# Optimization experiments

Hardware: AMD Instinct MI355X
Metric: run time of the kernel (lower is better)

Reference implementation:

```python
import jax, jax.numpy as jnp
import numpy as np

V_MIN = -10.0
V_MAX = 10.0
N_ATOMS = 101
LN_EPS = 1e-5

B = 131072
N_OBS = 60
N_ACT = 20
H = 256


def _layer_norm(x, g, b):
    mu = jnp.mean(x, axis=-1, keepdims=True)
    var = jnp.mean(jnp.square(x - mu), axis=-1, keepdims=True)
    return (x - mu) * jax.lax.rsqrt(var + LN_EPS) * g + b


def _mlp(x, W1, b1, g1, be1, W2, b2, g2, be2, W3, b3, g3, be3, W4, b4):
    h = jax.nn.silu(_layer_norm(x @ W1 + b1, g1, be1))
    h = jax.nn.silu(_layer_norm(h @ W2 + b2, g2, be2))
    h = jax.nn.silu(_layer_norm(h @ W3 + b3, g3, be3))
    return h @ W4 + b4  # [B, N_ATOMS] logits


def setup_inputs() -> dict:
    key = jax.random.key(0)
    ks = jax.random.split(key, 10)
    s = 0.05
    return {
        'obs': jax.random.normal(ks[0], (B, N_OBS), jnp.float32),
        'actions': jax.random.normal(ks[1], (B, N_ACT), jnp.float32),
        'rewards': jax.random.normal(ks[2], (B,), jnp.float32),
        'bootstrap': jax.random.uniform(ks[3], (B,), jnp.float32),
        'discount': jax.random.uniform(ks[4], (B,), jnp.float32, 0.95, 0.99),
        'q_support': jnp.linspace(V_MIN, V_MAX, N_ATOMS, dtype=jnp.float32),
        'W1': jax.random.normal(ks[5], (N_OBS + N_ACT, H), jnp.float32) * s,
        'b1': jnp.zeros((H,), jnp.float32),
        'g1': jnp.ones((H,), jnp.float32),
        'be1': jnp.zeros((H,), jnp.float32),
        'W2': jax.random.normal(ks[6], (H, H // 2), jnp.float32) * s,
        'b2': jnp.zeros((H // 2,), jnp.float32),
        'g2': jnp.ones((H // 2,), jnp.float32),
        'be2': jnp.zeros((H // 2,), jnp.float32),
        'W3': jax.random.normal(ks[7], (H // 2, H // 4), jnp.float32) * s,
        'b3': jnp.zeros((H // 4,), jnp.float32),
        'g3': jnp.ones((H // 4,), jnp.float32),
        'be3': jnp.zeros((H // 4,), jnp.float32),
        'W4': jax.random.normal(ks[8], (H // 4, N_ATOMS), jnp.float32) * s,
        'b4': jnp.zeros((N_ATOMS,), jnp.float32),
    }


def reference(obs, actions, rewards, bootstrap, discount, q_support,
              W1, b1, g1, be1, W2, b2, g2, be2, W3, b3, g3, be3, W4, b4):
    batch = rewards.shape[0]
    delta_z = (V_MAX - V_MIN) / (N_ATOMS - 1)
    # Bellman target support: [B, N_ATOMS]
    target_z = rewards[:, None] + bootstrap[:, None] * discount[:, None] * q_support
    target_z = jnp.clip(target_z, V_MIN, V_MAX)
    b = (target_z - V_MIN) / delta_z
    li = jnp.floor(b).astype(jnp.int32)
    ui = jnp.ceil(b).astype(jnp.int32)
    is_int = ui == li
    lower_mask = is_int & (li > 0)
    upper_mask = is_int & (li == 0)
    li = jnp.where(lower_mask, li - 1, li)
    ui = jnp.where(upper_mask, ui + 1, ui)
    lf = li.astype(b.dtype)
    uf = ui.astype(b.dtype)

    x = jnp.concatenate([obs, actions], axis=-1)
    logits = _mlp(x, W1, b1, g1, be1, W2, b2, g2, be2, W3, b3, g3, be3, W4, b4)
    next_dist = jax.nn.softmax(logits, axis=1)

    size = batch * N_ATOMS
    offset = (jnp.arange(batch, dtype=jnp.int32) * N_ATOMS)[:, None]
    l_idx = jnp.clip((li + offset).reshape(-1), 0, size - 1)
    u_idx = jnp.clip((ui + offset).reshape(-1), 0, size - 1)
    lw = (next_dist * (uf - b)).reshape(-1)
    uw = (next_dist * (b - lf)).reshape(-1)
    proj = jnp.zeros((size,), next_dist.dtype).at[l_idx].add(lw).at[u_idx].add(uw)
    return proj.reshape(batch, N_ATOMS)
```

## Files before the change

kernel.cpp:

```cpp
#include <hip/hip_runtime.h>
#include <math.h>

typedef __bf16 bf16x8 __attribute__((ext_vector_type(8)));
typedef float f32x4 __attribute__((ext_vector_type(4)));

__global__ void conv_weights(const float* __restrict__ W1, const float* __restrict__ W2,
                             const float* __restrict__ W3, const float* __restrict__ W4,
                             __bf16* __restrict__ ws)
{
  const int f = blockIdx.x * 4 + (threadIdx.x >> 6);
  const int lane = threadIdx.x & 63;
  int f0, ntot, Ksrc, Nsrc, off;
  const float* W;
  if (f < 48)       { f0 = f;       ntot = 16; Ksrc = 80;  Nsrc = 256; W = W1; off = 0; }
  else if (f < 112) { f0 = f - 48;  ntot = 8;  Ksrc = 256; Nsrc = 128; W = W2; off = 24576; }
  else if (f < 128) { f0 = f - 112; ntot = 4;  Ksrc = 128; Nsrc = 64;  W = W3; off = 57344; }
  else              { f0 = f - 128; ntot = 8;  Ksrc = 64;  Nsrc = 101; W = W4; off = 65536; }
  const int kt = f0 / ntot, nt = f0 % ntot;
  const int q = lane >> 4, c = lane & 15;
  const int n = nt * 16 + c;
  bf16x8 v;
#pragma unroll
  for (int j = 0; j < 8; ++j) {
    const int k = kt * 32 + q * 8 + j;
    const float x = (k < Ksrc && n < Nsrc) ? W[k * Nsrc + n] : 0.f;
    v[j] = (__bf16)x;
  }
  ((bf16x8*)(ws + off))[f0 * 64 + lane] = v;
}


__global__ __launch_bounds__(256, 3)
void sacq_wave(const float* __restrict__ obs,  const float* __restrict__ act,
               const float* __restrict__ rew,  const float* __restrict__ boot,
               const float* __restrict__ disc, const float* __restrict__ qsup,
               const float* __restrict__ b1, const float* __restrict__ g1, const float* __restrict__ be1,
               const float* __restrict__ b2, const float* __restrict__ g2, const float* __restrict__ be2,
               const float* __restrict__ b3, const float* __restrict__ g3, const float* __restrict__ be3,
               const float* __restrict__ b4,
               const __bf16* __restrict__ ws,
               float* __restrict__ out)
{
  __shared__ float sm[8768];
  const int t = threadIdx.x;
  const int wv = t >> 6, lane = t & 63;
  const int q = lane >> 4, c = lane & 15;
  float* smw = sm + wv * 2192;
  __bf16* h1 = (__bf16*)smw;
  __bf16* h2 = (__bf16*)smw;
  __bf16* h3 = (__bf16*)smw;
  float*  proj = smw + 576;
  const int row0w = blockIdx.x * 64 + wv * 16;
  const bf16x8* wsf = (const bf16x8*)ws;

  f32x4 acc1[16];
  {
    bf16x8 A1[3];
    const float4* ob4 = (const float4*)(obs + (size_t)(row0w + c) * 60);
    const float4* ac4 = (const float4*)(act + (size_t)(row0w + c) * 20);
#pragma unroll
    for (int kt = 0; kt < 3; ++kt) {
      const int k0 = kt * 32 + q * 8;
      float v[8];
      if (k0 < 56) {
        const float4 a = ob4[k0 / 4], b = ob4[k0 / 4 + 1];
        v[0]=a.x; v[1]=a.y; v[2]=a.z; v[3]=a.w; v[4]=b.x; v[5]=b.y; v[6]=b.z; v[7]=b.w;
      } else if (k0 == 56) {
        const float4 a = ob4[14], b = ac4[0];
        v[0]=a.x; v[1]=a.y; v[2]=a.z; v[3]=a.w; v[4]=b.x; v[5]=b.y; v[6]=b.z; v[7]=b.w;
      } else if (k0 < 80) {
        const float4 a = ac4[(k0 - 60) / 4], b = ac4[(k0 - 60) / 4 + 1];
        v[0]=a.x; v[1]=a.y; v[2]=a.z; v[3]=a.w; v[4]=b.x; v[5]=b.y; v[6]=b.z; v[7]=b.w;
      } else {
#pragma unroll
        for (int j = 0; j < 8; ++j) v[j] = 0.f;
      }
#pragma unroll
      for (int j = 0; j < 8; ++j) A1[kt][j] = (__bf16)v[j];
    }
#pragma unroll
    for (int nt = 0; nt < 16; ++nt) {
      const float bb = b1[nt * 16 + c];
      f32x4 vv = {bb, bb, bb, bb};
      acc1[nt] = vv;
    }
#pragma unroll
    for (int ch = 0; ch < 4; ++ch) {
      bf16x8 Bb[3][4];
#pragma unroll
      for (int kt = 0; kt < 3; ++kt)
#pragma unroll
        for (int j = 0; j < 4; ++j)
          Bb[kt][j] = wsf[(kt * 16 + ch * 4 + j) * 64 + lane];
#pragma unroll
      for (int kt = 0; kt < 3; ++kt)
#pragma unroll
        for (int j = 0; j < 4; ++j)
          acc1[ch * 4 + j] = __builtin_amdgcn_mfma_f32_16x16x32_bf16(A1[kt], Bb[kt][j], acc1[ch * 4 + j], 0, 0, 0);
    }
    float mu[4], rs[4];
#pragma unroll
    for (int r = 0; r < 4; ++r) {
      float s = 0.f, s2 = 0.f;
#pragma unroll
      for (int nt = 0; nt < 16; ++nt) { const float v = acc1[nt][r]; s += v; s2 += v * v; }
      s += __shfl_xor(s, 1); s2 += __shfl_xor(s2, 1);
      s += __shfl_xor(s, 2); s2 += __shfl_xor(s2, 2);
      s += __shfl_xor(s, 4); s2 += __shfl_xor(s2, 4);
      s += __shfl_xor(s, 8); s2 += __shfl_xor(s2, 8);
      const float m = s * (1.f / 256.f);
      mu[r] = m;
      rs[r] = rsqrtf(s2 * (1.f / 256.f) - m * m + 1e-5f);
    }
#pragma unroll
    for (int nt = 0; nt < 16; ++nt) {
      const int col = nt * 16 + c;
      const float gg = g1[col], bb = be1[col];
#pragma unroll
      for (int r = 0; r < 4; ++r) {
        float v = (acc1[nt][r] - mu[r]) * rs[r] * gg + bb;
        v = v * __builtin_amdgcn_rcpf(1.f + __expf(-v));
        h1[(4 * q + r) * 264 + col] = (__bf16)v;
      }
    }
  }

  {
    f32x4 acc2[8];
#pragma unroll
    for (int nt = 0; nt < 8; ++nt) {
      const float bb = b2[nt * 16 + c];
      f32x4 vv = {bb, bb, bb, bb};
      acc2[nt] = vv;
    }
    bf16x8 B2[3][8];
#pragma unroll
    for (int nt = 0; nt < 8; ++nt) B2[0][nt] = wsf[3072 + (0 * 8 + nt) * 64 + lane];
#pragma unroll
    for (int nt = 0; nt < 8; ++nt) B2[1][nt] = wsf[3072 + (1 * 8 + nt) * 64 + lane];
#pragma unroll
    for (int kt = 0; kt < 8; ++kt) {
      if (kt + 2 < 8) {
#pragma unroll
        for (int nt = 0; nt < 8; ++nt)
          B2[(kt + 2) % 3][nt] = wsf[3072 + ((kt + 2) * 8 + nt) * 64 + lane];
      }
      const bf16x8 A2 = *(const bf16x8*)(h1 + c * 264 + kt * 32 + q * 8);
#pragma unroll
      for (int nt = 0; nt < 8; ++nt)
        acc2[nt] = __builtin_amdgcn_mfma_f32_16x16x32_bf16(A2, B2[kt % 3][nt], acc2[nt], 0, 0, 0);
    }
    float mu[4], rs[4];
#pragma unroll
    for (int r = 0; r < 4; ++r) {
      float s = 0.f, s2 = 0.f;
#pragma unroll
      for (int nt = 0; nt < 8; ++nt) { const float v = acc2[nt][r]; s += v; s2 += v * v; }
      s += __shfl_xor(s, 1); s2 += __shfl_xor(s2, 1);
      s += __shfl_xor(s, 2); s2 += __shfl_xor(s2, 2);
      s += __shfl_xor(s, 4); s2 += __shfl_xor(s2, 4);
      s += __shfl_xor(s, 8); s2 += __shfl_xor(s2, 8);
      const float m = s * (1.f / 128.f);
      mu[r] = m;
      rs[r] = rsqrtf(s2 * (1.f / 128.f) - m * m + 1e-5f);
    }
#pragma unroll
    for (int nt = 0; nt < 8; ++nt) {
      const int col = nt * 16 + c;
      const float gg = g2[col], bb = be2[col];
#pragma unroll
      for (int r = 0; r < 4; ++r) {
        float v = (acc2[nt][r] - mu[r]) * rs[r] * gg + bb;
        v = v * __builtin_amdgcn_rcpf(1.f + __expf(-v));
        h2[(4 * q + r) * 136 + col] = (__bf16)v;
      }
    }
  }

  {
    bf16x8 B3[4][4];
#pragma unroll
    for (int kt = 0; kt < 4; ++kt)
#pragma unroll
      for (int nt = 0; nt < 4; ++nt)
        B3[kt][nt] = wsf[7168 + (kt * 4 + nt) * 64 + lane];
    f32x4 acc3[4];
#pragma unroll
    for (int nt = 0; nt < 4; ++nt) {
      const float bb = b3[nt * 16 + c];
      f32x4 vv = {bb, bb, bb, bb};
      acc3[nt] = vv;
    }
#pragma unroll
    for (int kt = 0; kt < 4; ++kt) {
      const bf16x8 A3 = *(const bf16x8*)(h2 + c * 136 + kt * 32 + q * 8);
#pragma unroll
      for (int nt = 0; nt < 4; ++nt)
        acc3[nt] = __builtin_amdgcn_mfma_f32_16x16x32_bf16(A3, B3[kt][nt], acc3[nt], 0, 0, 0);
    }
    float mu[4], rs[4];
#pragma unroll
    for (int r = 0; r < 4; ++r) {
      float s = 0.f, s2 = 0.f;
#pragma unroll
      for (int nt = 0; nt < 4; ++nt) { const float v = acc3[nt][r]; s += v; s2 += v * v; }
      s += __shfl_xor(s, 1); s2 += __shfl_xor(s2, 1);
      s += __shfl_xor(s, 2); s2 += __shfl_xor(s2, 2);
      s += __shfl_xor(s, 4); s2 += __shfl_xor(s2, 4);
      s += __shfl_xor(s, 8); s2 += __shfl_xor(s2, 8);
      const float m = s * (1.f / 64.f);
      mu[r] = m;
      rs[r] = rsqrtf(s2 * (1.f / 64.f) - m * m + 1e-5f);
    }
#pragma unroll
    for (int nt = 0; nt < 4; ++nt) {
      const int col = nt * 16 + c;
      const float gg = g3[col], bb = be3[col];
#pragma unroll
      for (int r = 0; r < 4; ++r) {
        float v = (acc3[nt][r] - mu[r]) * rs[r] * gg + bb;
        v = v * __builtin_amdgcn_rcpf(1.f + __expf(-v));
        h3[(4 * q + r) * 72 + col] = (__bf16)v;
      }
    }
  }

  {
    bf16x8 B4[2][7];
#pragma unroll
    for (int kt = 0; kt < 2; ++kt)
#pragma unroll
      for (int nt = 0; nt < 7; ++nt)
        B4[kt][nt] = wsf[8192 + (kt * 8 + nt) * 64 + lane];
    bf16x8 A4f[2];
#pragma unroll
    for (int kt = 0; kt < 2; ++kt)
      A4f[kt] = *(const bf16x8*)(h3 + c * 72 + kt * 32 + q * 8);

    asm volatile("" ::: "memory");
    {
      f32x4 z = {0.f, 0.f, 0.f, 0.f};
      f32x4* p4 = (f32x4*)proj;
      for (int i = lane; i < 404; i += 64) p4[i] = z;
    }

    f32x4 a4[7];
#pragma unroll
    for (int nt = 0; nt < 7; ++nt) {
      const int col = nt * 16 + c;
      const float bb = (col < 101) ? b4[col] : 0.f;
      f32x4 vv = {bb, bb, bb, bb};
      a4[nt] = vv;
    }
#pragma unroll
    for (int kt = 0; kt < 2; ++kt) {
#pragma unroll
      for (int nt = 0; nt < 7; ++nt)
        a4[nt] = __builtin_amdgcn_mfma_f32_16x16x32_bf16(A4f[kt], B4[kt][nt], a4[nt], 0, 0, 0);
    }

    float mx4[4] = {-3.4e38f, -3.4e38f, -3.4e38f, -3.4e38f};
#pragma unroll
    for (int nt = 0; nt < 7; ++nt) {
      const bool ok = (nt < 6) | (c < 5);
#pragma unroll
      for (int r = 0; r < 4; ++r)
        if (ok) mx4[r] = fmaxf(mx4[r], a4[nt][r]);
    }
#pragma unroll
    for (int r = 0; r < 4; ++r) {
      mx4[r] = fmaxf(mx4[r], __shfl_xor(mx4[r], 1));
      mx4[r] = fmaxf(mx4[r], __shfl_xor(mx4[r], 2));
      mx4[r] = fmaxf(mx4[r], __shfl_xor(mx4[r], 4));
      mx4[r] = fmaxf(mx4[r], __shfl_xor(mx4[r], 8));
    }
    float sm4[4] = {0.f, 0.f, 0.f, 0.f};
#pragma unroll
    for (int nt = 0; nt < 7; ++nt) {
      const bool ok = (nt < 6) | (c < 5);
#pragma unroll
      for (int r = 0; r < 4; ++r) {
        const float e = ok ? __expf(a4[nt][r] - mx4[r]) : 0.f;
        a4[nt][r] = e;
        sm4[r] += e;
      }
    }
    float inv4[4];
#pragma unroll
    for (int r = 0; r < 4; ++r) {
      float s = sm4[r];
      s += __shfl_xor(s, 1);
      s += __shfl_xor(s, 2);
      s += __shfl_xor(s, 4);
      s += __shfl_xor(s, 8);
      inv4[r] = __builtin_amdgcn_rcpf(s);
    }

    float rwv[4], bdv[4];
#pragma unroll
    for (int r = 0; r < 4; ++r) {
      const int gr = row0w + 4 * q + r;
      rwv[r] = rew[gr];
      bdv[r] = boot[gr] * disc[gr];
    }

#pragma unroll
    for (int nt = 0; nt < 7; ++nt) {
      const int col = nt * 16 + c;
      if ((nt < 6) | (c < 5)) {
        const float qsv = qsup[col];
#pragma unroll
        for (int r = 0; r < 4; ++r) {
          const float p = a4[nt][r] * inv4[r];
          float tz = rwv[r] + bdv[r] * qsv;
          tz = fminf(fmaxf(tz, -10.f), 10.f);
          const float b_ = (tz + 10.f) * 5.f;
          const float fl = floorf(b_), cl = ceilf(b_);
          int li = (int)fl, ui = (int)cl;
          if (ui == li) { if (li > 0) --li; else ++ui; }
          const int rb = (4 * q + r) * 101;
          atomicAdd(&proj[rb + li], p * ((float)ui - b_));
          atomicAdd(&proj[rb + ui], p * (b_ - (float)li));
        }
      }
    }
  }

  {
    const f32x4* p4 = (const f32x4*)proj;
    f32x4* o4 = (f32x4*)(out + (size_t)row0w * 101);
    for (int i = lane; i < 404; i += 64) o4[i] = p4[i];
  }
}

extern "C" void kernel_launch(void* const* d_in, const int* in_sizes, int n_in,
                              void* d_out, int out_size, void* d_ws, size_t ws_size,
                              hipStream_t stream)
{
  const int B = in_sizes[2];
  __bf16* ws = (__bf16*)d_ws;

  conv_weights<<<dim3(36), dim3(256), 0, stream>>>(
      (const float*)d_in[6], (const float*)d_in[10], (const float*)d_in[14],
      (const float*)d_in[18], ws);

  sacq_wave<<<dim3(B / 64), dim3(256), 0, stream>>>(
      (const float*)d_in[0],  (const float*)d_in[1],  (const float*)d_in[2],
      (const float*)d_in[3],  (const float*)d_in[4],  (const float*)d_in[5],
      (const float*)d_in[7],  (const float*)d_in[8],  (const float*)d_in[9],
      (const float*)d_in[11], (const float*)d_in[12], (const float*)d_in[13],
      (const float*)d_in[15], (const float*)d_in[16], (const float*)d_in[17],
      (const float*)d_in[19], ws, (float*)d_out);
}
```

Baseline: 323.2 us.

## Transpose MFMA accumulators through LDS for vectorized LayerNorm/SiLU/softmax epilogues

Each wave now spills its MFMA accumulator tiles into a per-wave LDS scratch buffer in a transposed layout. Lanes then reread them so each lane handles four rows of one column, with mean and rstd shared through LDS, instead of each lane covering four rows across many column tiles. The bias, gamma, beta and q_support vectors are packed into the workspace by an extra block of the weight-conversion kernel, and rewards, bootstrap and discount are read as float4. The aim is to cut register pressure and per-element broadcast loads in the epilogues. The cost is LDS traffic, a doubled shared-memory footprint and a drop of the launch-bounds occupancy hint from 3 to 2 blocks per CU.

```diff
diff --git a/kernel.cpp b/kernel.cpp
--- a/kernel.cpp
+++ b/kernel.cpp
@@ -6,8 +6,32 @@
 
 __global__ void conv_weights(const float* __restrict__ W1, const float* __restrict__ W2,
                              const float* __restrict__ W3, const float* __restrict__ W4,
+                             const float* __restrict__ b1, const float* __restrict__ g1, const float* __restrict__ be1,
+                             const float* __restrict__ b2, const float* __restrict__ g2, const float* __restrict__ be2,
+                             const float* __restrict__ b3, const float* __restrict__ g3, const float* __restrict__ be3,
+                             const float* __restrict__ b4, const float* __restrict__ qsup,
                              __bf16* __restrict__ ws)
 {
+  if (blockIdx.x == 36) {
+    float* Pp = (float*)(ws + 73728);
+    const int t = threadIdx.x;
+    Pp[t]       = b1[t];
+    Pp[256 + t] = g1[t];
+    Pp[512 + t] = be1[t];
+    if (t < 128) {
+      Pp[768 + t]  = b2[t];
+      Pp[896 + t]  = g2[t];
+      Pp[1024 + t] = be2[t];
+      Pp[1344 + t] = (t < 101) ? b4[t]   : 0.f;
+      Pp[1472 + t] = (t < 101) ? qsup[t] : 0.f;
+    }
+    if (t < 64) {
+      Pp[1152 + t] = b3[t];
+      Pp[1216 + t] = g3[t];
+      Pp[1280 + t] = be3[t];
+    }
+    return;
+  }
   const int f = blockIdx.x * 4 + (threadIdx.x >> 6);
   const int lane = threadIdx.x & 63;
   int f0, ntot, Ksrc, Nsrc, off;
@@ -30,7 +54,7 @@
 }
 
 
-__global__ __launch_bounds__(256, 3)
+__global__ __launch_bounds__(256, 2)
 void sacq_wave(const float* __restrict__ obs,  const float* __restrict__ act,
                const float* __restrict__ rew,  const float* __restrict__ boot,
                const float* __restrict__ disc, const float* __restrict__ qsup,
@@ -41,17 +65,21 @@
                const __bf16* __restrict__ ws,
                float* __restrict__ out)
 {
-  __shared__ float sm[8768];
+  __shared__ float sm[16960];
   const int t = threadIdx.x;
   const int wv = t >> 6, lane = t & 63;
   const int q = lane >> 4, c = lane & 15;
-  float* smw = sm + wv * 2192;
-  __bf16* h1 = (__bf16*)smw;
-  __bf16* h2 = (__bf16*)smw;
-  __bf16* h3 = (__bf16*)smw;
-  float*  proj = smw + 576;
+  float* smw = sm + wv * 4240;
+  float* scr = smw;
+  __bf16* h = (__bf16*)(smw + 2048);
+  float* muL = smw + 4160;
+  float* rsL = smw + 4176;
+  float* proj = smw + 2624;
   const int row0w = blockIdx.x * 64 + wv * 16;
   const bf16x8* wsf = (const bf16x8*)ws;
+  const float* Pp = (const float*)(const void*)(ws + 73728);
+  const int lq = lane >> 2;
+  const int lr = (lane & 3) * 4;
 
   f32x4 acc1[16];
   {
@@ -80,7 +108,7 @@
     }
 #pragma unroll
     for (int nt = 0; nt < 16; ++nt) {
-      const float bb = b1[nt * 16 + c];
+      const float bb = Pp[nt * 16 + c];
       f32x4 vv = {bb, bb, bb, bb};
       acc1[nt] = vv;
     }
@@ -98,29 +126,39 @@
         for (int j = 0; j < 4; ++j)
           acc1[ch * 4 + j] = __builtin_amdgcn_mfma_f32_16x16x32_bf16(A1[kt], Bb[kt][j], acc1[ch * 4 + j], 0, 0, 0);
     }
-    float mu[4], rs[4];
+    float s[4] = {0.f,0.f,0.f,0.f}, s2[4] = {0.f,0.f,0.f,0.f};
+#pragma unroll
+    for (int nt = 0; nt < 16; ++nt)
+#pragma unroll
+      for (int r = 0; r < 4; ++r) { const float v = acc1[nt][r]; s[r] += v; s2[r] += v * v; }
 #pragma unroll
     for (int r = 0; r < 4; ++r) {
-      float s = 0.f, s2 = 0.f;
-#pragma unroll
-      for (int nt = 0; nt < 16; ++nt) { const float v = acc1[nt][r]; s += v; s2 += v * v; }
-      s += __shfl_xor(s, 1); s2 += __shfl_xor(s2, 1);
-      s += __shfl_xor(s, 2); s2 += __shfl_xor(s2, 2);
-      s += __shfl_xor(s, 4); s2 += __shfl_xor(s2, 4);
-      s += __shfl_xor(s, 8); s2 += __shfl_xor(s2, 8);
-      const float m = s * (1.f / 256.f);
-      mu[r] = m;
-      rs[r] = rsqrtf(s2 * (1.f / 256.f) - m * m + 1e-5f);
-    }
-#pragma unroll
-    for (int nt = 0; nt < 16; ++nt) {
-      const int col = nt * 16 + c;
-      const float gg = g1[col], bb = be1[col];
-#pragma unroll
-      for (int r = 0; r < 4; ++r) {
-        float v = (acc1[nt][r] - mu[r]) * rs[r] * gg + bb;
-        v = v * __builtin_amdgcn_rcpf(1.f + __expf(-v));
-        h1[(4 * q + r) * 264 + col] = (__bf16)v;
+      s[r] += __shfl_xor(s[r], 1); s2[r] += __shfl_xor(s2[r], 1);
+      s[r] += __shfl_xor(s[r], 2); s2[r] += __shfl_xor(s2[r], 2);
+      s[r] += __shfl_xor(s[r], 4); s2[r] += __shfl_xor(s2[r], 4);
+      s[r] += __shfl_xor(s[r], 8); s2[r] += __shfl_xor(s2[r], 8);
+      const float m = s[r] * (1.f / 256.f);
+      const float rv = rsqrtf(s2[r] * (1.f / 256.f) - m * m + 1e-5f);
+      if (c == 0) { muL[4 * q + r] = m; rsL[4 * q + r] = rv; }
+    }
+#pragma unroll
+    for (int hh = 0; hh < 2; ++hh) {
+#pragma unroll
+      for (int ntl = 0; ntl < 8; ++ntl)
+        *(f32x4*)(scr + (ntl * 16 + c) * 16 + 4 * q) = acc1[hh * 8 + ntl];
+#pragma unroll 1
+      for (int it = 0; it < 8; ++it) {
+        const int colh = it * 16 + lq, col = hh * 128 + colh;
+        const f32x4 v  = *(const f32x4*)(scr + colh * 16 + lr);
+        const f32x4 m  = *(const f32x4*)(muL + lr);
+        const f32x4 rv = *(const f32x4*)(rsL + lr);
+        const float gg = Pp[256 + col], bb = Pp[512 + col];
+#pragma unroll
+        for (int j = 0; j < 4; ++j) {
+          float x = (v[j] - m[j]) * rv[j] * gg + bb;
+          x = x * __builtin_amdgcn_rcpf(1.f + __expf(-x));
+          h[(lr + j) * 264 + col] = (__bf16)x;
+        }
       }
     }
   }
@@ -129,7 +167,7 @@
     f32x4 acc2[8];
 #pragma unroll
     for (int nt = 0; nt < 8; ++nt) {
-      const float bb = b2[nt * 16 + c];
+      const float bb = Pp[768 + nt * 16 + c];
       f32x4 vv = {bb, bb, bb, bb};
       acc2[nt] = vv;
     }
@@ -145,34 +183,41 @@
         for (int nt = 0; nt < 8; ++nt)
           B2[(kt + 2) % 3][nt] = wsf[3072 + ((kt + 2) * 8 + nt) * 64 + lane];
       }
-      const bf16x8 A2 = *(const bf16x8*)(h1 + c * 264 + kt * 32 + q * 8);
+      const bf16x8 A2 = *(const bf16x8*)(h + c * 264 + kt * 32 + q * 8);
 #pragma unroll
       for (int nt = 0; nt < 8; ++nt)
         acc2[nt] = __builtin_amdgcn_mfma_f32_16x16x32_bf16(A2, B2[kt % 3][nt], acc2[nt], 0, 0, 0);
     }
-    float mu[4], rs[4];
+    float s[4] = {0.f,0.f,0.f,0.f}, s2[4] = {0.f,0.f,0.f,0.f};
+#pragma unroll
+    for (int nt = 0; nt < 8; ++nt)
+#pragma unroll
+      for (int r = 0; r < 4; ++r) { const float v = acc2[nt][r]; s[r] += v; s2[r] += v * v; }
 #pragma unroll
     for (int r = 0; r < 4; ++r) {
-      float s = 0.f, s2 = 0.f;
-#pragma unroll
-      for (int nt = 0; nt < 8; ++nt) { const float v = acc2[nt][r]; s += v; s2 += v * v; }
-      s += __shfl_xor(s, 1); s2 += __shfl_xor(s2, 1);
-      s += __shfl_xor(s, 2); s2 += __shfl_xor(s2, 2);
-      s += __shfl_xor(s, 4); s2 += __shfl_xor(s2, 4);
-      s += __shfl_xor(s, 8); s2 += __shfl_xor(s2, 8);
-      const float m = s * (1.f / 128.f);
-      mu[r] = m;
-      rs[r] = rsqrtf(s2 * (1.f / 128.f) - m * m + 1e-5f);
-    }
-#pragma unroll
-    for (int nt = 0; nt < 8; ++nt) {
-      const int col = nt * 16 + c;
-      const float gg = g2[col], bb = be2[col];
-#pragma unroll
-      for (int r = 0; r < 4; ++r) {
-        float v = (acc2[nt][r] - mu[r]) * rs[r] * gg + bb;
-        v = v * __builtin_amdgcn_rcpf(1.f + __expf(-v));
-        h2[(4 * q + r) * 136 + col] = (__bf16)v;
+      s[r] += __shfl_xor(s[r], 1); s2[r] += __shfl_xor(s2[r], 1);
+      s[r] += __shfl_xor(s[r], 2); s2[r] += __shfl_xor(s2[r], 2);
+      s[r] += __shfl_xor(s[r], 4); s2[r] += __shfl_xor(s2[r], 4);
+      s[r] += __shfl_xor(s[r], 8); s2[r] += __shfl_xor(s2[r], 8);
+      const float m = s[r] * (1.f / 128.f);
+      const float rv = rsqrtf(s2[r] * (1.f / 128.f) - m * m + 1e-5f);
+      if (c == 0) { muL[4 * q + r] = m; rsL[4 * q + r] = rv; }
+    }
+#pragma unroll
+    for (int nt = 0; nt < 8; ++nt)
+      *(f32x4*)(scr + (nt * 16 + c) * 16 + 4 * q) = acc2[nt];
+#pragma unroll 1
+    for (int it = 0; it < 8; ++it) {
+      const int col = it * 16 + lq;
+      const f32x4 v  = *(const f32x4*)(scr + col * 16 + lr);
+      const f32x4 m  = *(const f32x4*)(muL + lr);
+      const f32x4 rv = *(const f32x4*)(rsL + lr);
+      const float gg = Pp[896 + col], bb = Pp[1024 + col];
+#pragma unroll
+      for (int j = 0; j < 4; ++j) {
+        float x = (v[j] - m[j]) * rv[j] * gg + bb;
+        x = x * __builtin_amdgcn_rcpf(1.f + __expf(-x));
+        h[(lr + j) * 136 + col] = (__bf16)x;
       }
     }
   }
@@ -187,40 +232,47 @@
     f32x4 acc3[4];
 #pragma unroll
     for (int nt = 0; nt < 4; ++nt) {
-      const float bb = b3[nt * 16 + c];
+      const float bb = Pp[1152 + nt * 16 + c];
       f32x4 vv = {bb, bb, bb, bb};
       acc3[nt] = vv;
     }
 #pragma unroll
     for (int kt = 0; kt < 4; ++kt) {
-      const bf16x8 A3 = *(const bf16x8*)(h2 + c * 136 + kt * 32 + q * 8);
+      const bf16x8 A3 = *(const bf16x8*)(h + c * 136 + kt * 32 + q * 8);
 #pragma unroll
       for (int nt = 0; nt < 4; ++nt)
         acc3[nt] = __builtin_amdgcn_mfma_f32_16x16x32_bf16(A3, B3[kt][nt], acc3[nt], 0, 0, 0);
     }
-    float mu[4], rs[4];
+    float s[4] = {0.f,0.f,0.f,0.f}, s2[4] = {0.f,0.f,0.f,0.f};
+#pragma unroll
+    for (int nt = 0; nt < 4; ++nt)
+#pragma unroll
+      for (int r = 0; r < 4; ++r) { const float v = acc3[nt][r]; s[r] += v; s2[r] += v * v; }
 #pragma unroll
     for (int r = 0; r < 4; ++r) {
-      float s = 0.f, s2 = 0.f;
-#pragma unroll
-      for (int nt = 0; nt < 4; ++nt) { const float v = acc3[nt][r]; s += v; s2 += v * v; }
-      s += __shfl_xor(s, 1); s2 += __shfl_xor(s2, 1);
-      s += __shfl_xor(s, 2); s2 += __shfl_xor(s2, 2);
-      s += __shfl_xor(s, 4); s2 += __shfl_xor(s2, 4);
-      s += __shfl_xor(s, 8); s2 += __shfl_xor(s2, 8);
-      const float m = s * (1.f / 64.f);
-      mu[r] = m;
-      rs[r] = rsqrtf(s2 * (1.f / 64.f) - m * m + 1e-5f);
-    }
-#pragma unroll
-    for (int nt = 0; nt < 4; ++nt) {
-      const int col = nt * 16 + c;
-      const float gg = g3[col], bb = be3[col];
-#pragma unroll
-      for (int r = 0; r < 4; ++r) {
-        float v = (acc3[nt][r] - mu[r]) * rs[r] * gg + bb;
-        v = v * __builtin_amdgcn_rcpf(1.f + __expf(-v));
-        h3[(4 * q + r) * 72 + col] = (__bf16)v;
+      s[r] += __shfl_xor(s[r], 1); s2[r] += __shfl_xor(s2[r], 1);
+      s[r] += __shfl_xor(s[r], 2); s2[r] += __shfl_xor(s2[r], 2);
+      s[r] += __shfl_xor(s[r], 4); s2[r] += __shfl_xor(s2[r], 4);
+      s[r] += __shfl_xor(s[r], 8); s2[r] += __shfl_xor(s2[r], 8);
+      const float m = s[r] * (1.f / 64.f);
+      const float rv = rsqrtf(s2[r] * (1.f / 64.f) - m * m + 1e-5f);
+      if (c == 0) { muL[4 * q + r] = m; rsL[4 * q + r] = rv; }
+    }
+#pragma unroll
+    for (int nt = 0; nt < 4; ++nt)
+      *(f32x4*)(scr + (nt * 16 + c) * 16 + 4 * q) = acc3[nt];
+#pragma unroll 1
+    for (int it = 0; it < 4; ++it) {
+      const int col = it * 16 + lq;
+      const f32x4 v  = *(const f32x4*)(scr + col * 16 + lr);
+      const f32x4 m  = *(const f32x4*)(muL + lr);
+      const f32x4 rv = *(const f32x4*)(rsL + lr);
+      const float gg = Pp[1216 + col], bb = Pp[1280 + col];
+#pragma unroll
+      for (int j = 0; j < 4; ++j) {
+        float x = (v[j] - m[j]) * rv[j] * gg + bb;
+        x = x * __builtin_amdgcn_rcpf(1.f + __expf(-x));
+        h[(lr + j) * 72 + col] = (__bf16)x;
       }
     }
   }
@@ -235,7 +287,23 @@
     bf16x8 A4f[2];
 #pragma unroll
     for (int kt = 0; kt < 2; ++kt)
-      A4f[kt] = *(const bf16x8*)(h3 + c * 72 + kt * 32 + q * 8);
+      A4f[kt] = *(const bf16x8*)(h + c * 72 + kt * 32 + q * 8);
+    f32x4 a4[7];
+#pragma unroll
+    for (int nt = 0; nt < 7; ++nt) {
+      const float bb = Pp[1344 + nt * 16 + c];
+      f32x4 vv = {bb, bb, bb, bb};
+      a4[nt] = vv;
+    }
+#pragma unroll
+    for (int kt = 0; kt < 2; ++kt) {
+#pragma unroll
+      for (int nt = 0; nt < 7; ++nt)
+        a4[nt] = __builtin_amdgcn_mfma_f32_16x16x32_bf16(A4f[kt], B4[kt][nt], a4[nt], 0, 0, 0);
+    }
+#pragma unroll
+    for (int nt = 0; nt < 7; ++nt)
+      *(f32x4*)(scr + (nt * 16 + c) * 16 + 4 * q) = a4[nt];
 
     asm volatile("" ::: "memory");
     {
@@ -244,81 +312,66 @@
       for (int i = lane; i < 404; i += 64) p4[i] = z;
     }
 
-    f32x4 a4[7];
-#pragma unroll
-    for (int nt = 0; nt < 7; ++nt) {
-      const int col = nt * 16 + c;
-      const float bb = (col < 101) ? b4[col] : 0.f;
-      f32x4 vv = {bb, bb, bb, bb};
-      a4[nt] = vv;
-    }
-#pragma unroll
-    for (int kt = 0; kt < 2; ++kt) {
-#pragma unroll
-      for (int nt = 0; nt < 7; ++nt)
-        a4[nt] = __builtin_amdgcn_mfma_f32_16x16x32_bf16(A4f[kt], B4[kt][nt], a4[nt], 0, 0, 0);
-    }
-
-    float mx4[4] = {-3.4e38f, -3.4e38f, -3.4e38f, -3.4e38f};
-#pragma unroll
-    for (int nt = 0; nt < 7; ++nt) {
-      const bool ok = (nt < 6) | (c < 5);
-#pragma unroll
-      for (int r = 0; r < 4; ++r)
-        if (ok) mx4[r] = fmaxf(mx4[r], a4[nt][r]);
-    }
-#pragma unroll
-    for (int r = 0; r < 4; ++r) {
-      mx4[r] = fmaxf(mx4[r], __shfl_xor(mx4[r], 1));
-      mx4[r] = fmaxf(mx4[r], __shfl_xor(mx4[r], 2));
-      mx4[r] = fmaxf(mx4[r], __shfl_xor(mx4[r], 4));
-      mx4[r] = fmaxf(mx4[r], __shfl_xor(mx4[r], 8));
-    }
-    float sm4[4] = {0.f, 0.f, 0.f, 0.f};
-#pragma unroll
-    for (int nt = 0; nt < 7; ++nt) {
-      const bool ok = (nt < 6) | (c < 5);
-#pragma unroll
-      for (int r = 0; r < 4; ++r) {
-        const float e = ok ? __expf(a4[nt][r] - mx4[r]) : 0.f;
-        a4[nt][r] = e;
-        sm4[r] += e;
-      }
-    }
-    float inv4[4];
-#pragma unroll
-    for (int r = 0; r < 4; ++r) {
-      float s = sm4[r];
-      s += __shfl_xor(s, 1);
-      s += __shfl_xor(s, 2);
-      s += __shfl_xor(s, 4);
-      s += __shfl_xor(s, 8);
-      inv4[r] = __builtin_amdgcn_rcpf(s);
-    }
-
-    float rwv[4], bdv[4];
-#pragma unroll
-    for (int r = 0; r < 4; ++r) {
-      const int gr = row0w + 4 * q + r;
-      rwv[r] = rew[gr];
-      bdv[r] = boot[gr] * disc[gr];
-    }
-
-#pragma unroll
-    for (int nt = 0; nt < 7; ++nt) {
-      const int col = nt * 16 + c;
-      if ((nt < 6) | (c < 5)) {
-        const float qsv = qsup[col];
-#pragma unroll
-        for (int r = 0; r < 4; ++r) {
-          const float p = a4[nt][r] * inv4[r];
-          float tz = rwv[r] + bdv[r] * qsv;
+    float mx[4] = {-3.4e38f, -3.4e38f, -3.4e38f, -3.4e38f};
+#pragma unroll 1
+    for (int it = 0; it < 7; ++it) {
+      const int col = it * 16 + lq;
+      const f32x4 v = *(const f32x4*)(scr + col * 16 + lr);
+      if (col < 101) {
+#pragma unroll
+        for (int j = 0; j < 4; ++j) mx[j] = fmaxf(mx[j], v[j]);
+      }
+    }
+#pragma unroll
+    for (int j = 0; j < 4; ++j) {
+      mx[j] = fmaxf(mx[j], __shfl_xor(mx[j], 4));
+      mx[j] = fmaxf(mx[j], __shfl_xor(mx[j], 8));
+      mx[j] = fmaxf(mx[j], __shfl_xor(mx[j], 16));
+      mx[j] = fmaxf(mx[j], __shfl_xor(mx[j], 32));
+    }
+    float sp[4] = {0.f, 0.f, 0.f, 0.f};
+#pragma unroll 1
+    for (int it = 0; it < 7; ++it) {
+      const int col = it * 16 + lq;
+      const f32x4 v = *(const f32x4*)(scr + col * 16 + lr);
+      const bool ok = col < 101;
+#pragma unroll
+      for (int j = 0; j < 4; ++j) sp[j] += ok ? __expf(v[j] - mx[j]) : 0.f;
+    }
+    float inv[4];
+#pragma unroll
+    for (int j = 0; j < 4; ++j) {
+      float x = sp[j];
+      x += __shfl_xor(x, 4);
+      x += __shfl_xor(x, 8);
+      x += __shfl_xor(x, 16);
+      x += __shfl_xor(x, 32);
+      inv[j] = __builtin_amdgcn_rcpf(x);
+    }
+
+    const f32x4 rw4 = *(const f32x4*)(rew  + row0w + lr);
+    const f32x4 bo4 = *(const f32x4*)(boot + row0w + lr);
+    const f32x4 di4 = *(const f32x4*)(disc + row0w + lr);
+    float bd[4];
+#pragma unroll
+    for (int j = 0; j < 4; ++j) bd[j] = bo4[j] * di4[j];
+
+#pragma unroll 1
+    for (int it = 0; it < 7; ++it) {
+      const int col = it * 16 + lq;
+      if (col < 101) {
+        const float qsv = Pp[1472 + col];
+        const f32x4 v = *(const f32x4*)(scr + col * 16 + lr);
+#pragma unroll
+        for (int j = 0; j < 4; ++j) {
+          const float p = __expf(v[j] - mx[j]) * inv[j];
+          float tz = rw4[j] + bd[j] * qsv;
           tz = fminf(fmaxf(tz, -10.f), 10.f);
           const float b_ = (tz + 10.f) * 5.f;
           const float fl = floorf(b_), cl = ceilf(b_);
           int li = (int)fl, ui = (int)cl;
           if (ui == li) { if (li > 0) --li; else ++ui; }
-          const int rb = (4 * q + r) * 101;
+          const int rb = (lr + j) * 101;
           atomicAdd(&proj[rb + li], p * ((float)ui - b_));
           atomicAdd(&proj[rb + ui], p * (b_ - (float)li));
         }
@@ -340,9 +393,13 @@
   const int B = in_sizes[2];
   __bf16* ws = (__bf16*)d_ws;
 
-  conv_weights<<<dim3(36), dim3(256), 0, stream>>>(
-      (const float*)d_in[6], (const float*)d_in[10], (const float*)d_in[14],
-      (const float*)d_in[18], ws);
+  conv_weights<<<dim3(37), dim3(256), 0, stream>>>(
+      (const float*)d_in[6],  (const float*)d_in[10], (const float*)d_in[14],
+      (const float*)d_in[18],
+      (const float*)d_in[7],  (const float*)d_in[8],  (const float*)d_in[9],
+      (const float*)d_in[11], (const float*)d_in[12], (const float*)d_in[13],
+      (const float*)d_in[15], (const float*)d_in[16], (const float*)d_in[17],
+      (const float*)d_in[19], (const float*)d_in[5],  ws);
 
   sacq_wave<<<dim3(B / 64), dim3(256), 0, stream>>>(
       (const float*)d_in[0],  (const float*)d_in[1],  (const float*)d_in[2],
```

Result: slower. 344.9 us (+6.7%).

## Process two 16-row tiles per wave to reuse weight fragments across rows

Applied to the files above, without the earlier changes.

Each wave now handles 32 rows (two 16-row MFMA tiles), so every weight B-fragment loaded from global memory feeds two MFMAs, which halves weight traffic per row. Bias, LayerNorm and q_support parameters are packed into the workspace by an extra block of the prep kernel. Reward, bootstrap and discount are read as vectors. LDS per block doubles, register pressure rises and launch bounds drop to 2 blocks per CU, so occupancy and latency hiding may suffer.

```diff
diff --git a/kernel.cpp b/kernel.cpp
--- a/kernel.cpp
+++ b/kernel.cpp
@@ -6,8 +6,32 @@
 
 __global__ void conv_weights(const float* __restrict__ W1, const float* __restrict__ W2,
                              const float* __restrict__ W3, const float* __restrict__ W4,
+                             const float* __restrict__ b1, const float* __restrict__ g1, const float* __restrict__ be1,
+                             const float* __restrict__ b2, const float* __restrict__ g2, const float* __restrict__ be2,
+                             const float* __restrict__ b3, const float* __restrict__ g3, const float* __restrict__ be3,
+                             const float* __restrict__ b4, const float* __restrict__ qsup,
                              __bf16* __restrict__ ws)
 {
+  if (blockIdx.x == 36) {
+    float* Pp = (float*)(ws + 73728);
+    const int t = threadIdx.x;
+    Pp[t]       = b1[t];
+    Pp[256 + t] = g1[t];
+    Pp[512 + t] = be1[t];
+    if (t < 128) {
+      Pp[768 + t]  = b2[t];
+      Pp[896 + t]  = g2[t];
+      Pp[1024 + t] = be2[t];
+      Pp[1344 + t] = (t < 101) ? b4[t]   : 0.f;
+      Pp[1472 + t] = (t < 101) ? qsup[t] : 0.f;
+    }
+    if (t < 64) {
+      Pp[1152 + t] = b3[t];
+      Pp[1216 + t] = g3[t];
+      Pp[1280 + t] = be3[t];
+    }
+    return;
+  }
   const int f = blockIdx.x * 4 + (threadIdx.x >> 6);
   const int lane = threadIdx.x & 63;
   int f0, ntot, Ksrc, Nsrc, off;
@@ -30,7 +54,7 @@
 }
 
 
-__global__ __launch_bounds__(256, 3)
+__global__ __launch_bounds__(256, 2)
 void sacq_wave(const float* __restrict__ obs,  const float* __restrict__ act,
                const float* __restrict__ rew,  const float* __restrict__ boot,
                const float* __restrict__ disc, const float* __restrict__ qsup,
@@ -41,48 +65,51 @@
                const __bf16* __restrict__ ws,
                float* __restrict__ out)
 {
-  __shared__ float sm[8768];
+  __shared__ float sm[17536];
   const int t = threadIdx.x;
   const int wv = t >> 6, lane = t & 63;
   const int q = lane >> 4, c = lane & 15;
-  float* smw = sm + wv * 2192;
-  __bf16* h1 = (__bf16*)smw;
-  __bf16* h2 = (__bf16*)smw;
-  __bf16* h3 = (__bf16*)smw;
-  float*  proj = smw + 576;
-  const int row0w = blockIdx.x * 64 + wv * 16;
+  float* smw = sm + wv * 4384;
+  __bf16* h = (__bf16*)smw;
+  float* proj = smw + 1152;
+  const int row0w = blockIdx.x * 128 + wv * 32;
   const bf16x8* wsf = (const bf16x8*)ws;
-
-  f32x4 acc1[16];
+  const float* Pp = (const float*)(const void*)(ws + 73728);
+
+  f32x4 acc1[2][16];
   {
-    bf16x8 A1[3];
-    const float4* ob4 = (const float4*)(obs + (size_t)(row0w + c) * 60);
-    const float4* ac4 = (const float4*)(act + (size_t)(row0w + c) * 20);
-#pragma unroll
-    for (int kt = 0; kt < 3; ++kt) {
-      const int k0 = kt * 32 + q * 8;
-      float v[8];
-      if (k0 < 56) {
-        const float4 a = ob4[k0 / 4], b = ob4[k0 / 4 + 1];
-        v[0]=a.x; v[1]=a.y; v[2]=a.z; v[3]=a.w; v[4]=b.x; v[5]=b.y; v[6]=b.z; v[7]=b.w;
-      } else if (k0 == 56) {
-        const float4 a = ob4[14], b = ac4[0];
-        v[0]=a.x; v[1]=a.y; v[2]=a.z; v[3]=a.w; v[4]=b.x; v[5]=b.y; v[6]=b.z; v[7]=b.w;
-      } else if (k0 < 80) {
-        const float4 a = ac4[(k0 - 60) / 4], b = ac4[(k0 - 60) / 4 + 1];
-        v[0]=a.x; v[1]=a.y; v[2]=a.z; v[3]=a.w; v[4]=b.x; v[5]=b.y; v[6]=b.z; v[7]=b.w;
-      } else {
-#pragma unroll
-        for (int j = 0; j < 8; ++j) v[j] = 0.f;
-      }
-#pragma unroll
-      for (int j = 0; j < 8; ++j) A1[kt][j] = (__bf16)v[j];
+    bf16x8 A1[2][3];
+#pragma unroll
+    for (int rt = 0; rt < 2; ++rt) {
+      const float4* ob4 = (const float4*)(obs + (size_t)(row0w + rt * 16 + c) * 60);
+      const float4* ac4 = (const float4*)(act + (size_t)(row0w + rt * 16 + c) * 20);
+#pragma unroll
+      for (int kt = 0; kt < 3; ++kt) {
+        const int k0 = kt * 32 + q * 8;
+        float v[8];
+        if (k0 < 56) {
+          const float4 a = ob4[k0 / 4], b = ob4[k0 / 4 + 1];
+          v[0]=a.x; v[1]=a.y; v[2]=a.z; v[3]=a.w; v[4]=b.x; v[5]=b.y; v[6]=b.z; v[7]=b.w;
+        } else if (k0 == 56) {
+          const float4 a = ob4[14], b = ac4[0];
+          v[0]=a.x; v[1]=a.y; v[2]=a.z; v[3]=a.w; v[4]=b.x; v[5]=b.y; v[6]=b.z; v[7]=b.w;
+        } else if (k0 < 80) {
+          const float4 a = ac4[(k0 - 60) / 4], b = ac4[(k0 - 60) / 4 + 1];
+          v[0]=a.x; v[1]=a.y; v[2]=a.z; v[3]=a.w; v[4]=b.x; v[5]=b.y; v[6]=b.z; v[7]=b.w;
+        } else {
+#pragma unroll
+          for (int j = 0; j < 8; ++j) v[j] = 0.f;
+        }
+#pragma unroll
+        for (int j = 0; j < 8; ++j) A1[rt][kt][j] = (__bf16)v[j];
+      }
     }
 #pragma unroll
     for (int nt = 0; nt < 16; ++nt) {
-      const float bb = b1[nt * 16 + c];
+      const float bb = Pp[nt * 16 + c];
       f32x4 vv = {bb, bb, bb, bb};
-      acc1[nt] = vv;
+      acc1[0][nt] = vv;
+      acc1[1][nt] = vv;
     }
 #pragma unroll
     for (int ch = 0; ch < 4; ++ch) {
@@ -96,83 +123,99 @@
       for (int kt = 0; kt < 3; ++kt)
 #pragma unroll
         for (int j = 0; j < 4; ++j)
-          acc1[ch * 4 + j] = __builtin_amdgcn_mfma_f32_16x16x32_bf16(A1[kt], Bb[kt][j], acc1[ch * 4 + j], 0, 0, 0);
-    }
-    float mu[4], rs[4];
-#pragma unroll
-    for (int r = 0; r < 4; ++r) {
-      float s = 0.f, s2 = 0.f;
-#pragma unroll
-      for (int nt = 0; nt < 16; ++nt) { const float v = acc1[nt][r]; s += v; s2 += v * v; }
-      s += __shfl_xor(s, 1); s2 += __shfl_xor(s2, 1);
-      s += __shfl_xor(s, 2); s2 += __shfl_xor(s2, 2);
-      s += __shfl_xor(s, 4); s2 += __shfl_xor(s2, 4);
-      s += __shfl_xor(s, 8); s2 += __shfl_xor(s2, 8);
-      const float m = s * (1.f / 256.f);
-      mu[r] = m;
-      rs[r] = rsqrtf(s2 * (1.f / 256.f) - m * m + 1e-5f);
-    }
-#pragma unroll
-    for (int nt = 0; nt < 16; ++nt) {
-      const int col = nt * 16 + c;
-      const float gg = g1[col], bb = be1[col];
+#pragma unroll
+          for (int rt = 0; rt < 2; ++rt)
+            acc1[rt][ch * 4 + j] = __builtin_amdgcn_mfma_f32_16x16x32_bf16(A1[rt][kt], Bb[kt][j], acc1[rt][ch * 4 + j], 0, 0, 0);
+    }
+#pragma unroll
+    for (int rt = 0; rt < 2; ++rt) {
+      float s[4] = {0.f,0.f,0.f,0.f}, s2[4] = {0.f,0.f,0.f,0.f};
+#pragma unroll
+      for (int nt = 0; nt < 16; ++nt)
+#pragma unroll
+        for (int r = 0; r < 4; ++r) { const float v = acc1[rt][nt][r]; s[r] += v; s2[r] += v * v; }
+      float mu[4], rs[4];
 #pragma unroll
       for (int r = 0; r < 4; ++r) {
-        float v = (acc1[nt][r] - mu[r]) * rs[r] * gg + bb;
-        v = v * __builtin_amdgcn_rcpf(1.f + __expf(-v));
-        h1[(4 * q + r) * 264 + col] = (__bf16)v;
+        s[r] += __shfl_xor(s[r], 1); s2[r] += __shfl_xor(s2[r], 1);
+        s[r] += __shfl_xor(s[r], 2); s2[r] += __shfl_xor(s2[r], 2);
+        s[r] += __shfl_xor(s[r], 4); s2[r] += __shfl_xor(s2[r], 4);
+        s[r] += __shfl_xor(s[r], 8); s2[r] += __shfl_xor(s2[r], 8);
+        const float m = s[r] * (1.f / 256.f);
+        mu[r] = m;
+        rs[r] = rsqrtf(s2[r] * (1.f / 256.f) - m * m + 1e-5f);
+      }
+#pragma unroll
+      for (int nt = 0; nt < 16; ++nt) {
+        const int col = nt * 16 + c;
+        const float gg = Pp[256 + col], bb = Pp[512 + col];
+#pragma unroll
+        for (int r = 0; r < 4; ++r) {
+          float v = (acc1[rt][nt][r] - mu[r]) * rs[r] * gg + bb;
+          v = v * __builtin_amdgcn_rcpf(1.f + __expf(-v));
+          h[(rt * 16 + 4 * q + r) * 264 + col] = (__bf16)v;
+        }
       }
     }
   }
 
   {
-    f32x4 acc2[8];
+    f32x4 acc2[2][8];
 #pragma unroll
     for (int nt = 0; nt < 8; ++nt) {
-      const float bb = b2[nt * 16 + c];
+      const float bb = Pp[768 + nt * 16 + c];
       f32x4 vv = {bb, bb, bb, bb};
-      acc2[nt] = vv;
-    }
-    bf16x8 B2[3][8];
-#pragma unroll
-    for (int nt = 0; nt < 8; ++nt) B2[0][nt] = wsf[3072 + (0 * 8 + nt) * 64 + lane];
-#pragma unroll
-    for (int nt = 0; nt < 8; ++nt) B2[1][nt] = wsf[3072 + (1 * 8 + nt) * 64 + lane];
+      acc2[0][nt] = vv;
+      acc2[1][nt] = vv;
+    }
+    bf16x8 B2[2][8];
+#pragma unroll
+    for (int nt = 0; nt < 8; ++nt) B2[0][nt] = wsf[3072 + nt * 64 + lane];
 #pragma unroll
     for (int kt = 0; kt < 8; ++kt) {
-      if (kt + 2 < 8) {
+      if (kt + 1 < 8) {
 #pragma unroll
         for (int nt = 0; nt < 8; ++nt)
-          B2[(kt + 2) % 3][nt] = wsf[3072 + ((kt + 2) * 8 + nt) * 64 + lane];
-      }
-      const bf16x8 A2 = *(const bf16x8*)(h1 + c * 264 + kt * 32 + q * 8);
+          B2[(kt + 1) & 1][nt] = wsf[3072 + ((kt + 1) * 8 + nt) * 64 + lane];
+      }
+      bf16x8 A2r[2];
+#pragma unroll
+      for (int rt = 0; rt < 2; ++rt)
+        A2r[rt] = *(const bf16x8*)(h + (rt * 16 + c) * 264 + kt * 32 + q * 8);
 #pragma unroll
       for (int nt = 0; nt < 8; ++nt)
-        acc2[nt] = __builtin_amdgcn_mfma_f32_16x16x32_bf16(A2, B2[kt % 3][nt], acc2[nt], 0, 0, 0);
-    }
-    float mu[4], rs[4];
-#pragma unroll
-    for (int r = 0; r < 4; ++r) {
-      float s = 0.f, s2 = 0.f;
-#pragma unroll
-      for (int nt = 0; nt < 8; ++nt) { const float v = acc2[nt][r]; s += v; s2 += v * v; }
-      s += __shfl_xor(s, 1); s2 += __shfl_xor(s2, 1);
-      s += __shfl_xor(s, 2); s2 += __shfl_xor(s2, 2);
-      s += __shfl_xor(s, 4); s2 += __shfl_xor(s2, 4);
-      s += __shfl_xor(s, 8); s2 += __shfl_xor(s2, 8);
-      const float m = s * (1.f / 128.f);
-      mu[r] = m;
-      rs[r] = rsqrtf(s2 * (1.f / 128.f) - m * m + 1e-5f);
-    }
-#pragma unroll
-    for (int nt = 0; nt < 8; ++nt) {
-      const int col = nt * 16 + c;
-      const float gg = g2[col], bb = be2[col];
+#pragma unroll
+        for (int rt = 0; rt < 2; ++rt)
+          acc2[rt][nt] = __builtin_amdgcn_mfma_f32_16x16x32_bf16(A2r[rt], B2[kt & 1][nt], acc2[rt][nt], 0, 0, 0);
+    }
+#pragma unroll
+    for (int rt = 0; rt < 2; ++rt) {
+      float s[4] = {0.f,0.f,0.f,0.f}, s2[4] = {0.f,0.f,0.f,0.f};
+#pragma unroll
+      for (int nt = 0; nt < 8; ++nt)
+#pragma unroll
+        for (int r = 0; r < 4; ++r) { const float v = acc2[rt][nt][r]; s[r] += v; s2[r] += v * v; }
+      float mu[4], rs[4];
 #pragma unroll
       for (int r = 0; r < 4; ++r) {
-        float v = (acc2[nt][r] - mu[r]) * rs[r] * gg + bb;
-        v = v * __builtin_amdgcn_rcpf(1.f + __expf(-v));
-        h2[(4 * q + r) * 136 + col] = (__bf16)v;
+        s[r] += __shfl_xor(s[r], 1); s2[r] += __shfl_xor(s2[r], 1);
+        s[r] += __shfl_xor(s[r], 2); s2[r] += __shfl_xor(s2[r], 2);
+        s[r] += __shfl_xor(s[r], 4); s2[r] += __shfl_xor(s2[r], 4);
+        s[r] += __shfl_xor(s[r], 8); s2[r] += __shfl_xor(s2[r], 8);
+        const float m = s[r] * (1.f / 128.f);
+        mu[r] = m;
+        rs[r] = rsqrtf(s2[r] * (1.f / 128.f) - m * m + 1e-5f);
+      }
+#pragma unroll
+      for (int nt = 0; nt < 8; ++nt) {
+        const int col = nt * 16 + c;
+        const float gg = Pp[896 + col], bb = Pp[1024 + col];
+#pragma unroll
+        for (int r = 0; r < 4; ++r) {
+          float v = (acc2[rt][nt][r] - mu[r]) * rs[r] * gg + bb;
+          v = v * __builtin_amdgcn_rcpf(1.f + __expf(-v));
+          h[(rt * 16 + 4 * q + r) * 136 + col] = (__bf16)v;
+        }
       }
     }
   }
@@ -184,43 +227,54 @@
 #pragma unroll
       for (int nt = 0; nt < 4; ++nt)
         B3[kt][nt] = wsf[7168 + (kt * 4 + nt) * 64 + lane];
-    f32x4 acc3[4];
+    f32x4 acc3[2][4];
 #pragma unroll
     for (int nt = 0; nt < 4; ++nt) {
-      const float bb = b3[nt * 16 + c];
+      const float bb = Pp[1152 + nt * 16 + c];
       f32x4 vv = {bb, bb, bb, bb};
-      acc3[nt] = vv;
+      acc3[0][nt] = vv;
+      acc3[1][nt] = vv;
     }
 #pragma unroll
     for (int kt = 0; kt < 4; ++kt) {
-      const bf16x8 A3 = *(const bf16x8*)(h2 + c * 136 + kt * 32 + q * 8);
+      bf16x8 A3r[2];
+#pragma unroll
+      for (int rt = 0; rt < 2; ++rt)
+        A3r[rt] = *(const bf16x8*)(h + (rt * 16 + c) * 136 + kt * 32 + q * 8);
 #pragma unroll
       for (int nt = 0; nt < 4; ++nt)
-        acc3[nt] = __builtin_amdgcn_mfma_f32_16x16x32_bf16(A3, B3[kt][nt], acc3[nt], 0, 0, 0);
-    }
-    float mu[4], rs[4];
-#pragma unroll
-    for (int r = 0; r < 4; ++r) {
-      float s = 0.f, s2 = 0.f;
-#pragma unroll
-      for (int nt = 0; nt < 4; ++nt) { const float v = acc3[nt][r]; s += v; s2 += v * v; }
-      s += __shfl_xor(s, 1); s2 += __shfl_xor(s2, 1);
-      s += __shfl_xor(s, 2); s2 += __shfl_xor(s2, 2);
-      s += __shfl_xor(s, 4); s2 += __shfl_xor(s2, 4);
-      s += __shfl_xor(s, 8); s2 += __shfl_xor(s2, 8);
-      const float m = s * (1.f / 64.f);
-      mu[r] = m;
-      rs[r] = rsqrtf(s2 * (1.f / 64.f) - m * m + 1e-5f);
-    }
-#pragma unroll
-    for (int nt = 0; nt < 4; ++nt) {
-      const int col = nt * 16 + c;
-      const float gg = g3[col], bb = be3[col];
+#pragma unroll
+        for (int rt = 0; rt < 2; ++rt)
+          acc3[rt][nt] = __builtin_amdgcn_mfma_f32_16x16x32_bf16(A3r[rt], B3[kt][nt], acc3[rt][nt], 0, 0, 0);
+    }
+#pragma unroll
+    for (int rt = 0; rt < 2; ++rt) {
+      float s[4] = {0.f,0.f,0.f,0.f}, s2[4] = {0.f,0.f,0.f,0.f};
+#pragma unroll
+      for (int nt = 0; nt < 4; ++nt)
+#pragma unroll
+        for (int r = 0; r < 4; ++r) { const float v = acc3[rt][nt][r]; s[r] += v; s2[r] += v * v; }
+      float mu[4], rs[4];
 #pragma unroll
       for (int r = 0; r < 4; ++r) {
-        float v = (acc3[nt][r] - mu[r]) * rs[r] * gg + bb;
-        v = v * __builtin_amdgcn_rcpf(1.f + __expf(-v));
-        h3[(4 * q + r) * 72 + col] = (__bf16)v;
+        s[r] += __shfl_xor(s[r], 1); s2[r] += __shfl_xor(s2[r], 1);
+        s[r] += __shfl_xor(s[r], 2); s2[r] += __shfl_xor(s2[r], 2);
+        s[r] += __shfl_xor(s[r], 4); s2[r] += __shfl_xor(s2[r], 4);
+        s[r] += __shfl_xor(s[r], 8); s2[r] += __shfl_xor(s2[r], 8);
+        const float m = s[r] * (1.f / 64.f);
+        mu[r] = m;
+        rs[r] = rsqrtf(s2[r] * (1.f / 64.f) - m * m + 1e-5f);
+      }
+#pragma unroll
+      for (int nt = 0; nt < 4; ++nt) {
+        const int col = nt * 16 + c;
+        const float gg = Pp[1216 + col], bb = Pp[1280 + col];
+#pragma unroll
+        for (int r = 0; r < 4; ++r) {
+          float v = (acc3[rt][nt][r] - mu[r]) * rs[r] * gg + bb;
+          v = v * __builtin_amdgcn_rcpf(1.f + __expf(-v));
+          h[(rt * 16 + 4 * q + r) * 72 + col] = (__bf16)v;
+        }
       }
     }
   }
@@ -232,95 +286,100 @@
 #pragma unroll
       for (int nt = 0; nt < 7; ++nt)
         B4[kt][nt] = wsf[8192 + (kt * 8 + nt) * 64 + lane];
-    bf16x8 A4f[2];
-#pragma unroll
-    for (int kt = 0; kt < 2; ++kt)
-      A4f[kt] = *(const bf16x8*)(h3 + c * 72 + kt * 32 + q * 8);
+    bf16x8 A4f[2][2];
+#pragma unroll
+    for (int rt = 0; rt < 2; ++rt)
+#pragma unroll
+      for (int kt = 0; kt < 2; ++kt)
+        A4f[rt][kt] = *(const bf16x8*)(h + (rt * 16 + c) * 72 + kt * 32 + q * 8);
 
     asm volatile("" ::: "memory");
     {
       f32x4 z = {0.f, 0.f, 0.f, 0.f};
       f32x4* p4 = (f32x4*)proj;
-      for (int i = lane; i < 404; i += 64) p4[i] = z;
-    }
-
-    f32x4 a4[7];
+      for (int i = lane; i < 808; i += 64) p4[i] = z;
+    }
+
+    f32x4 a4[2][7];
 #pragma unroll
     for (int nt = 0; nt < 7; ++nt) {
-      const int col = nt * 16 + c;
-      const float bb = (col < 101) ? b4[col] : 0.f;
+      const float bb = Pp[1344 + nt * 16 + c];
       f32x4 vv = {bb, bb, bb, bb};
-      a4[nt] = vv;
-    }
-#pragma unroll
-    for (int kt = 0; kt < 2; ++kt) {
+      a4[0][nt] = vv;
+      a4[1][nt] = vv;
+    }
+#pragma unroll
+    for (int kt = 0; kt < 2; ++kt)
 #pragma unroll
       for (int nt = 0; nt < 7; ++nt)
-        a4[nt] = __builtin_amdgcn_mfma_f32_16x16x32_bf16(A4f[kt], B4[kt][nt], a4[nt], 0, 0, 0);
-    }
-
-    float mx4[4] = {-3.4e38f, -3.4e38f, -3.4e38f, -3.4e38f};
-#pragma unroll
-    for (int nt = 0; nt < 7; ++nt) {
-      const bool ok = (nt < 6) | (c < 5);
-#pragma unroll
-      for (int r = 0; r < 4; ++r)
-        if (ok) mx4[r] = fmaxf(mx4[r], a4[nt][r]);
-    }
-#pragma unroll
-    for (int r = 0; r < 4; ++r) {
-      mx4[r] = fmaxf(mx4[r], __shfl_xor(mx4[r], 1));
-      mx4[r] = fmaxf(mx4[r], __shfl_xor(mx4[r], 2));
-      mx4[r] = fmaxf(mx4[r], __shfl_xor(mx4[r], 4));
-      mx4[r] = fmaxf(mx4[r], __shfl_xor(mx4[r], 8));
-    }
-    float sm4[4] = {0.f, 0.f, 0.f, 0.f};
-#pragma unroll
-    for (int nt = 0; nt < 7; ++nt) {
-      const bool ok = (nt < 6) | (c < 5);
+#pragma unroll
+        for (int rt = 0; rt < 2; ++rt)
+          a4[rt][nt] = __builtin_amdgcn_mfma_f32_16x16x32_bf16(A4f[rt][kt], B4[kt][nt], a4[rt][nt], 0, 0, 0);
+
+#pragma unroll
+    for (int rt = 0; rt < 2; ++rt) {
+      float mx4[4] = {-3.4e38f, -3.4e38f, -3.4e38f, -3.4e38f};
+#pragma unroll
+      for (int nt = 0; nt < 7; ++nt) {
+        const bool ok = (nt < 6) | (c < 5);
+#pragma unroll
+        for (int r = 0; r < 4; ++r)
+          if (ok) mx4[r] = fmaxf(mx4[r], a4[rt][nt][r]);
+      }
 #pragma unroll
       for (int r = 0; r < 4; ++r) {
-        const float e = ok ? __expf(a4[nt][r] - mx4[r]) : 0.f;
-        a4[nt][r] = e;
-        sm4[r] += e;
-      }
-    }
-    float inv4[4];
-#pragma unroll
-    for (int r = 0; r < 4; ++r) {
-      float s = sm4[r];
-      s += __shfl_xor(s, 1);
-      s += __shfl_xor(s, 2);
-      s += __shfl_xor(s, 4);
-      s += __shfl_xor(s, 8);
-      inv4[r] = __builtin_amdgcn_rcpf(s);
-    }
-
-    float rwv[4], bdv[4];
-#pragma unroll
-    for (int r = 0; r < 4; ++r) {
-      const int gr = row0w + 4 * q + r;
-      rwv[r] = rew[gr];
-      bdv[r] = boot[gr] * disc[gr];
-    }
-
-#pragma unroll
-    for (int nt = 0; nt < 7; ++nt) {
-      const int col = nt * 16 + c;
-      if ((nt < 6) | (c < 5)) {
-        const float qsv = qsup[col];
+        mx4[r] = fmaxf(mx4[r], __shfl_xor(mx4[r], 1));
+        mx4[r] = fmaxf(mx4[r], __shfl_xor(mx4[r], 2));
+        mx4[r] = fmaxf(mx4[r], __shfl_xor(mx4[r], 4));
+        mx4[r] = fmaxf(mx4[r], __shfl_xor(mx4[r], 8));
+      }
+      float sm4[4] = {0.f, 0.f, 0.f, 0.f};
+#pragma unroll
+      for (int nt = 0; nt < 7; ++nt) {
+        const bool ok = (nt < 6) | (c < 5);
 #pragma unroll
         for (int r = 0; r < 4; ++r) {
-          const float p = a4[nt][r] * inv4[r];
-          float tz = rwv[r] + bdv[r] * qsv;
-          tz = fminf(fmaxf(tz, -10.f), 10.f);
-          const float b_ = (tz + 10.f) * 5.f;
-          const float fl = floorf(b_), cl = ceilf(b_);
-          int li = (int)fl, ui = (int)cl;
-          if (ui == li) { if (li > 0) --li; else ++ui; }
-          const int rb = (4 * q + r) * 101;
-          atomicAdd(&proj[rb + li], p * ((float)ui - b_));
-          atomicAdd(&proj[rb + ui], p * (b_ - (float)li));
+          const float e = ok ? __expf(a4[rt][nt][r] - mx4[r]) : 0.f;
+          a4[rt][nt][r] = e;
+          sm4[r] += e;
+        }
+      }
+      float inv4[4];
+#pragma unroll
+      for (int r = 0; r < 4; ++r) {
+        float s = sm4[r];
+        s += __shfl_xor(s, 1);
+        s += __shfl_xor(s, 2);
+        s += __shfl_xor(s, 4);
+        s += __shfl_xor(s, 8);
+        inv4[r] = __builtin_amdgcn_rcpf(s);
+      }
+
+      const f32x4 rw4 = *(const f32x4*)(rew  + row0w + rt * 16 + 4 * q);
+      const f32x4 bo4 = *(const f32x4*)(boot + row0w + rt * 16 + 4 * q);
+      const f32x4 di4 = *(const f32x4*)(disc + row0w + rt * 16 + 4 * q);
+      float bd[4];
+#pragma unroll
+      for (int r = 0; r < 4; ++r) bd[r] = bo4[r] * di4[r];
+
+#pragma unroll
+      for (int nt = 0; nt < 7; ++nt) {
+        const int col = nt * 16 + c;
+        if ((nt < 6) | (c < 5)) {
+          const float qsv = Pp[1472 + col];
+#pragma unroll
+          for (int r = 0; r < 4; ++r) {
+            const float p = a4[rt][nt][r] * inv4[r];
+            float tz = rw4[r] + bd[r] * qsv;
+            tz = fminf(fmaxf(tz, -10.f), 10.f);
+            const float b_ = (tz + 10.f) * 5.f;
+            const float fl = floorf(b_), cl = ceilf(b_);
+            int li = (int)fl, ui = (int)cl;
+            if (ui == li) { if (li > 0) --li; else ++ui; }
+            const int rb = (rt * 16 + 4 * q + r) * 101;
+            atomicAdd(&proj[rb + li], p * ((float)ui - b_));
+            atomicAdd(&proj[rb + ui], p * (b_ - (float)li));
+          }
         }
       }
     }
@@ -329,7 +388,7 @@
   {
     const f32x4* p4 = (const f32x4*)proj;
     f32x4* o4 = (f32x4*)(out + (size_t)row0w * 101);
-    for (int i = lane; i < 404; i += 64) o4[i] = p4[i];
+    for (int i = lane; i < 808; i += 64) o4[i] = p4[i];
   }
 }
 
@@ -340,11 +399,15 @@
   const int B = in_sizes[2];
   __bf16* ws = (__bf16*)d_ws;
 
-  conv_weights<<<dim3(36), dim3(256), 0, stream>>>(
-      (const float*)d_in[6], (const float*)d_in[10], (const float*)d_in[14],
-      (const float*)d_in[18], ws);
-
-  sacq_wave<<<dim3(B / 64), dim3(256), 0, stream>>>(
+  conv_weights<<<dim3(37), dim3(256), 0, stream>>>(
+      (const float*)d_in[6],  (const float*)d_in[10], (const float*)d_in[14],
+      (const float*)d_in[18],
+      (const float*)d_in[7],  (const float*)d_in[8],  (const float*)d_in[9],
+      (const float*)d_in[11], (const float*)d_in[12], (const float*)d_in[13],
+      (const float*)d_in[15], (const float*)d_in[16], (const float*)d_in[17],
+      (const float*)d_in[19], (const float*)d_in[5],  ws);
+
+  sacq_wave<<<dim3(B / 128), dim3(256), 0, stream>>>(
       (const float*)d_in[0],  (const float*)d_in[1],  (const float*)d_in[2],
       (const float*)d_in[3],  (const float*)d_in[4],  (const float*)d_in[5],
       (const float*)d_in[7],  (const float*)d_in[8],  (const float*)d_in[9],
```

Result: slower. 332.7 us (+2.9%).
